# Kernel optimization log

Hardware: AMD Instinct MI355X
Metric: run time of the kernel (lower is better)

Reference implementation:

```python
import jax, jax.numpy as jnp
import numpy as np

H = 12           # num heads
ALPHA = 0.8      # mixing coefficient
OT_EPS = 1.0     # Sinkhorn epsilon
MAX_ITER = 50    # Sinkhorn iterations (reference runs full loop; torch may early-exit after convergence)
NEG = -1e9


def _l2norm(x, eps=1e-12):
    # matches torch.nn.functional.normalize(dim=-1)
    n = jnp.sqrt(jnp.sum(x * x, axis=-1, keepdims=True))
    return x / jnp.maximum(n, eps)


def setup_inputs() -> dict:
    rng = jax.random.key(0)
    ks = jax.random.split(rng, 12)
    B, L, D = 2, 2048, 768
    dk = D // H
    f = jnp.float32
    return {
        "query": jax.random.normal(ks[0], (B, L, D), dtype=f),
        "key": jax.random.normal(ks[1], (B, L, D), dtype=f),
        "short": jax.random.normal(ks[2], (B, H, L, L), dtype=f),
        "aspect": jax.random.normal(ks[3], (B, D), dtype=f),
        "mask": jnp.ones((B, 1, L), dtype=jnp.int32),
        "Wq": jax.random.normal(ks[4], (D, D), dtype=f) * (1.0 / np.sqrt(D)),
        "bq": jax.random.normal(ks[5], (D,), dtype=f) * 0.02,
        "Wk": jax.random.normal(ks[6], (D, D), dtype=f) * (1.0 / np.sqrt(D)),
        "bk": jax.random.normal(ks[7], (D,), dtype=f) * 0.02,
        "w_mu": jax.random.normal(ks[8], (dk, 1), dtype=f) * (1.0 / np.sqrt(dk)),
        "b_mu": jax.random.normal(ks[9], (1,), dtype=f) * 0.02,
        "bias_m": jax.random.normal(ks[10], (1,), dtype=f) * 0.02,
    }


def _forward(query, key, short, aspect, mask, Wq, bq, Wk, bk, w_mu, b_mu, bias_m):
    B, L, D = query.shape
    dk = D // H

    # unprojected head-split representations
    seq_h = query.reshape(B, L, H, dk).transpose(0, 2, 1, 3)       # [B,H,L,dk]
    asp_h = aspect.reshape(B, 1, H, dk).transpose(0, 2, 1, 3)      # [B,H,1,dk]

    m = mask[:, None, :, :]                                        # [B,1,1,L]

    q = (query @ Wq + bq).reshape(B, L, H, dk).transpose(0, 2, 1, 3)  # [B,H,L,dk]
    k = (key @ Wk + bk).reshape(B, L, H, dk).transpose(0, 2, 1, 3)    # [B,H,L,dk]

    scores = jnp.einsum('bhld,bhmd->bhlm', q, k) / np.sqrt(dk).astype(np.float32)
    scores = jnp.where(m == 0, NEG, scores)
    attn = jax.nn.softmax(scores + short, axis=-1)                 # [B,H,L,L]
    sentence_attn_output = jnp.einsum('bhlm,bhmd->bhld', attn, seq_h)

    # ---- Sinkhorn OT attention ----
    cos = jnp.sum(_l2norm(seq_h) * _l2norm(asp_h), axis=-1, keepdims=True)  # [B,H,L,1]
    cost = 1.0 - cos
    mu_logits = seq_h @ w_mu + b_mu                                # [B,H,L,1]
    m_t = jnp.transpose(m, (0, 1, 3, 2))                           # [B,1,L,1]
    mu_logits = jnp.where(m_t == 0, NEG, mu_logits)
    mu = jax.nn.softmax(mu_logits, axis=-2)                        # [B,H,L,1]
    nu = jax.nn.softmax(asp_h @ w_mu + b_mu, axis=-2)              # [B,H,1,1] (== 1)

    K = jnp.exp(-cost / OT_EPS)                                    # [B,H,L,1]

    def step(uv, _):
        u, v = uv
        u = mu / (K * v + 1e-8)                                    # K@v for [L,1]@[1,1]
        v = nu / (jnp.sum(K * u, axis=-2, keepdims=True) + 1e-8)   # K^T@u
        return (u, v), None

    (u, v), _ = jax.lax.scan(step, (jnp.ones_like(mu), jnp.ones_like(nu)), None, length=MAX_ITER)
    pi = u * K * v                                                 # [B,H,L,1]

    aspect_aware_rep = pi * seq_h                                  # [B,H,L,dk]
    out = ALPHA * sentence_attn_output + (1.0 - ALPHA) * aspect_aware_rep + bias_m
    return out                                                     # [B,H,L,dk]


def reference(query, key, short, aspect, mask, Wq, bq, Wk, bk, w_mu, b_mu, bias_m):
    return _forward(query, key, short, aspect, mask, Wq, bq, Wk, bk, w_mu, b_mu, bias_m)
```

## Files before the change

### kernel.cpp

```cpp
#include <hip/hip_runtime.h>
#include <math.h>

constexpr int NB = 2;
constexpr int NH = 12;
constexpr int SL = 2048;
constexpr int DM = 768;
constexpr int DK = 64;

typedef short s16x8 __attribute__((ext_vector_type(8)));
typedef float f32x4 __attribute__((ext_vector_type(4)));

__device__ inline unsigned short f2bf(float f) {
    unsigned int x = __float_as_uint(f);
    unsigned int r = (x + 0x7fffu + ((x >> 16) & 1u)) >> 16;
    return (unsigned short)r;
}
__device__ inline unsigned int pk2(float a, float b) {
    return (unsigned int)f2bf(a) | ((unsigned int)f2bf(b) << 16);
}

__global__ __launch_bounds__(256) void wt_cast(
    const float* __restrict__ W, unsigned short* __restrict__ Wt)
{
    __shared__ float t[64][65];
    const int k0 = blockIdx.x * 64, n0 = blockIdx.y * 64;
    const int tid = threadIdx.x;
    const int r = tid >> 2;
    const int c0 = (tid & 3) * 16;
#pragma unroll
    for (int j = 0; j < 4; ++j) {
        float4 v = *reinterpret_cast<const float4*>(
            &W[(size_t)(k0 + r) * DM + n0 + c0 + j * 4]);
        t[r][c0 + j*4 + 0] = v.x; t[r][c0 + j*4 + 1] = v.y;
        t[r][c0 + j*4 + 2] = v.z; t[r][c0 + j*4 + 3] = v.w;
    }
    __syncthreads();
    const int nr = tid >> 2, kc = (tid & 3) * 16;
    unsigned int o[8];
#pragma unroll
    for (int j = 0; j < 8; ++j)
        o[j] = pk2(t[kc + 2*j][nr], t[kc + 2*j + 1][nr]);
    unsigned short* dst = &Wt[(size_t)(n0 + nr) * DM + k0 + kc];
    uint4 a; a.x = o[0]; a.y = o[1]; a.z = o[2]; a.w = o[3];
    uint4 b; b.x = o[4]; b.y = o[5]; b.z = o[6]; b.w = o[7];
    *reinterpret_cast<uint4*>(dst) = a;
    *reinterpret_cast<uint4*>(dst + 8) = b;
}

__global__ __launch_bounds__(256) void proj_mfma(
    const float* __restrict__ X, const unsigned short* __restrict__ Wt,
    const float* __restrict__ bias, unsigned short* __restrict__ outw)
{
    __shared__ unsigned short Al[64 * 64];
    __shared__ unsigned short Bl[64 * 64];
    const int n0 = blockIdx.x * 64;
    const int m0 = blockIdx.y * 64;
    const int tid = threadIdx.x;
    const int w = tid >> 6, lane = tid & 63;
    const int lq = lane & 15, g = lane >> 4;
    const int msub = (w & 1) * 32, nsub = (w >> 1) * 32;

    const int srow = tid >> 2;
    const int sc = tid & 3;

    f32x4 acc[2][2];
#pragma unroll
    for (int i = 0; i < 2; ++i)
#pragma unroll
        for (int j = 0; j < 2; ++j) acc[i][j] = f32x4{0.f, 0.f, 0.f, 0.f};

    for (int k0 = 0; k0 < DM; k0 += 64) {
        const float* xp = &X[(size_t)(m0 + srow) * DM + k0 + sc * 8];
        float4 x0 = *reinterpret_cast<const float4*>(xp);
        float4 x1 = *reinterpret_cast<const float4*>(xp + 4);
        float4 x2 = *reinterpret_cast<const float4*>(xp + 32);
        float4 x3 = *reinterpret_cast<const float4*>(xp + 36);
        const unsigned short* wp = &Wt[(size_t)(n0 + srow) * DM + k0 + sc * 8];
        uint4 w0 = *reinterpret_cast<const uint4*>(wp);
        uint4 w1 = *reinterpret_cast<const uint4*>(wp + 32);
        __syncthreads();
        uint4 pa0, pa1;
        pa0.x = pk2(x0.x, x0.y); pa0.y = pk2(x0.z, x0.w);
        pa0.z = pk2(x1.x, x1.y); pa0.w = pk2(x1.z, x1.w);
        pa1.x = pk2(x2.x, x2.y); pa1.y = pk2(x2.z, x2.w);
        pa1.z = pk2(x3.x, x3.y); pa1.w = pk2(x3.z, x3.w);
        const int sw0 = (sc ^ (srow & 7)) << 3;
        const int sw1 = ((sc + 4) ^ (srow & 7)) << 3;
        *reinterpret_cast<uint4*>(&Al[srow * 64 + sw0]) = pa0;
        *reinterpret_cast<uint4*>(&Al[srow * 64 + sw1]) = pa1;
        *reinterpret_cast<uint4*>(&Bl[srow * 64 + sw0]) = w0;
        *reinterpret_cast<uint4*>(&Bl[srow * 64 + sw1]) = w1;
        __syncthreads();
#pragma unroll
        for (int ks = 0; ks < 2; ++ks) {
            s16x8 af[2], bfm[2];
#pragma unroll
            for (int ci = 0; ci < 2; ++ci) {
                const int row = nsub + ci * 16 + lq;
                af[ci] = *reinterpret_cast<const s16x8*>(
                    &Bl[row * 64 + (((4*ks + g) ^ (row & 7)) << 3)]);
            }
#pragma unroll
            for (int mi = 0; mi < 2; ++mi) {
                const int row = msub + mi * 16 + lq;
                bfm[mi] = *reinterpret_cast<const s16x8*>(
                    &Al[row * 64 + (((4*ks + g) ^ (row & 7)) << 3)]);
            }
#pragma unroll
            for (int ci = 0; ci < 2; ++ci)
#pragma unroll
                for (int mi = 0; mi < 2; ++mi)
                    acc[ci][mi] = __builtin_amdgcn_mfma_f32_16x16x32_bf16(
                        af[ci], bfm[mi], acc[ci][mi], 0, 0, 0);
        }
    }

    const int hh = blockIdx.x;
#pragma unroll
    for (int ci = 0; ci < 2; ++ci) {
        const int db = nsub + ci * 16 + g * 4;
        const float4 b4 = *reinterpret_cast<const float4*>(&bias[n0 + db]);
#pragma unroll
        for (int mi = 0; mi < 2; ++mi) {
            const int m = m0 + msub + mi * 16 + lq;
            const int b = m >> 11, l = m & 2047;
            uint2 uv;
            uv.x = pk2(acc[ci][mi][0] + b4.x, acc[ci][mi][1] + b4.y);
            uv.y = pk2(acc[ci][mi][2] + b4.z, acc[ci][mi][3] + b4.w);
            *reinterpret_cast<uint2*>(
                &outw[(((size_t)b * NH + hh) * SL + l) * DK + db]) = uv;
        }
    }
}

__device__ inline float block_sum(float v, float* red, int tid)
{
    __syncthreads();
#pragma unroll
    for (int o = 32; o > 0; o >>= 1) v += __shfl_down(v, o, 64);
    if ((tid & 63) == 0) red[tid >> 6] = v;
    __syncthreads();
    return red[0] + red[1] + red[2] + red[3];
}
__device__ inline float block_max(float v, float* red, int tid)
{
    __syncthreads();
#pragma unroll
    for (int o = 32; o > 0; o >>= 1) v = fmaxf(v, __shfl_down(v, o, 64));
    if ((tid & 63) == 0) red[tid >> 6] = v;
    __syncthreads();
    return fmaxf(fmaxf(red[0], red[1]), fmaxf(red[2], red[3]));
}

__global__ __launch_bounds__(256) void pi_kernel(
    const float* __restrict__ query, const float* __restrict__ aspect,
    const float* __restrict__ w_mu, const float* __restrict__ b_mu,
    float* __restrict__ pi_ws)
{
    const int bh = blockIdx.x;
    const int b = bh / NH, h = bh % NH;
    const int tid = threadIdx.x;

    __shared__ float red[4];
    __shared__ float wmu_s[DK];
    __shared__ float asp_s[DK];
    if (tid < DK) {
        wmu_s[tid] = w_mu[tid];
        asp_s[tid] = aspect[(size_t)b * DM + h * DK + tid];
    }
    __syncthreads();

    float an = 0.f;
#pragma unroll
    for (int d = 0; d < DK; ++d) an += asp_s[d] * asp_s[d];
    an = fmaxf(sqrtf(an), 1e-12f);

    float logit[8], Kv[8];
#pragma unroll
    for (int i = 0; i < 8; ++i) {
        const int l = tid + i * 256;
        const float4* x = reinterpret_cast<const float4*>(
            &query[((size_t)b * SL + l) * DM + h * DK]);
        float dot = 0.f, nn = 0.f, cs = 0.f;
#pragma unroll
        for (int d4 = 0; d4 < 16; ++d4) {
            const float4 xv = x[d4];
            dot += xv.x * wmu_s[d4*4+0] + xv.y * wmu_s[d4*4+1]
                 + xv.z * wmu_s[d4*4+2] + xv.w * wmu_s[d4*4+3];
            nn  += xv.x*xv.x + xv.y*xv.y + xv.z*xv.z + xv.w*xv.w;
            cs  += xv.x * asp_s[d4*4+0] + xv.y * asp_s[d4*4+1]
                 + xv.z * asp_s[d4*4+2] + xv.w * asp_s[d4*4+3];
        }
        const float n1 = fmaxf(sqrtf(nn), 1e-12f);
        const float cosv = cs / (n1 * an);
        logit[i] = dot + b_mu[0];
        Kv[i] = __expf(cosv - 1.0f);
    }

    float mx = logit[0];
#pragma unroll
    for (int i = 1; i < 8; ++i) mx = fmaxf(mx, logit[i]);
    const float gmax = block_max(mx, red, tid);

    float es[8]; float ps = 0.f;
#pragma unroll
    for (int i = 0; i < 8; ++i) { es[i] = __expf(logit[i] - gmax); ps += es[i]; }
    const float gsum = block_sum(ps, red, tid);

    float mu[8];
#pragma unroll
    for (int i = 0; i < 8; ++i) mu[i] = es[i] / gsum;

    float v = 1.f;
    float u[8] = {};
    for (int it = 0; it < 50; ++it) {
        float part = 0.f;
#pragma unroll
        for (int i = 0; i < 8; ++i) {
            u[i] = mu[i] / (Kv[i] * v + 1e-8f);
            part += Kv[i] * u[i];
        }
        const float S = block_sum(part, red, tid);
        v = 1.f / (S + 1e-8f);
    }

#pragma unroll
    for (int i = 0; i < 8; ++i) {
        const int l = tid + i * 256;
        pi_ws[(size_t)bh * SL + l] = u[i] * Kv[i] * v;
    }
}

__global__ __launch_bounds__(256) void flash_mfma(
    const unsigned short* __restrict__ q_ws,
    const unsigned short* __restrict__ k_ws,
    const float* __restrict__ query, const float* __restrict__ shortb,
    const float* __restrict__ pi_ws, const float* __restrict__ bias_m,
    float* __restrict__ out)
{
    __shared__ unsigned short Kl[64 * 64];
    __shared__ unsigned short Vt[64 * 64];

    const int bid = blockIdx.x;
    const int wg = (bid & 7) * 96 + (bid >> 3);
    const int bh = wg >> 5;
    const int qt = wg & 31;
    const int b = bh / NH, h = bh % NH;
    const int l0 = qt * 64;
    const int tid = threadIdx.x;
    const int w = tid >> 6, lane = tid & 63;
    const int lq = lane & 15, g = lane >> 4;
    const int qrow = l0 + w * 16 + lq;

    s16x8 qf0, qf1;
    {
        const unsigned short* qp = &q_ws[((size_t)bh * SL + qrow) * DK + g * 8];
        qf0 = *reinterpret_cast<const s16x8*>(qp);
        qf1 = *reinterpret_cast<const s16x8*>(qp + 32);
    }

    f32x4 acc[4];
#pragma unroll
    for (int d = 0; d < 4; ++d) acc[d] = f32x4{0.f, 0.f, 0.f, 0.f};
    float m_run = -1e30f, l_run = 0.f;

    const float* pshort = shortb + ((size_t)bh * SL + qrow) * SL;

    const int skey = tid >> 2, sc = tid & 3;
    const unsigned short* kgp =
        &k_ws[((size_t)bh * SL) * DK + skey * DK + sc * 8];
    unsigned short* kw0 = &Kl[skey * 64 + (((sc    ) ^ (skey & 7)) << 3)];
    unsigned short* kw1 = &Kl[skey * 64 + (((sc + 4) ^ (skey & 7)) << 3)];
    const int vkey = (tid & 31) * 2, vd0 = (tid >> 5) * 8;
    const float* vgp = &query[((size_t)b * SL) * DM + h * DK + vd0];

    auto stage = [&](int kt) {
        const unsigned short* kp = kgp + (size_t)kt * DK;
        uint4 ka = *reinterpret_cast<const uint4*>(kp);
        uint4 kb = *reinterpret_cast<const uint4*>(kp + 32);
        const float* vp = vgp + (size_t)(kt + vkey) * DM;
        float4 f0 = *reinterpret_cast<const float4*>(vp);
        float4 f1 = *reinterpret_cast<const float4*>(vp + 4);
        float4 f2 = *reinterpret_cast<const float4*>(vp + DM);
        float4 f3 = *reinterpret_cast<const float4*>(vp + DM + 4);
        __syncthreads();
        *reinterpret_cast<uint4*>(kw0) = ka;
        *reinterpret_cast<uint4*>(kw1) = kb;
        const float a0[8] = {f0.x,f0.y,f0.z,f0.w,f1.x,f1.y,f1.z,f1.w};
        const float a1[8] = {f2.x,f2.y,f2.z,f2.w,f3.x,f3.y,f3.z,f3.w};
#pragma unroll
        for (int j = 0; j < 8; ++j) {
            const int d = vd0 + j;
            *reinterpret_cast<unsigned int*>(
                &Vt[d * 64 + (vkey ^ ((d & 7) << 3))]) = pk2(a0[j], a1[j]);
        }
        __syncthreads();
    };

    auto compute = [&](const float4* shp) {
        f32x4 st[4];
#pragma unroll
        for (int s = 0; s < 4; ++s) {
            const int row = s * 16 + lq;
            const s16x8 ka0 = *reinterpret_cast<const s16x8*>(
                &Kl[row * 64 + (((g    ) ^ (row & 7)) << 3)]);
            const s16x8 ka1 = *reinterpret_cast<const s16x8*>(
                &Kl[row * 64 + (((4 + g) ^ (row & 7)) << 3)]);
            f32x4 c = {0.f, 0.f, 0.f, 0.f};
            c = __builtin_amdgcn_mfma_f32_16x16x32_bf16(ka0, qf0, c, 0, 0, 0);
            c = __builtin_amdgcn_mfma_f32_16x16x32_bf16(ka1, qf1, c, 0, 0, 0);
            st[s] = c;
        }
        float p[4][4];
        float tmax = -1e30f;
#pragma unroll
        for (int s = 0; s < 4; ++s) {
            const float* s4 = reinterpret_cast<const float*>(&shp[s]);
#pragma unroll
            for (int r = 0; r < 4; ++r) {
                const float sc_ = st[s][r] * 0.125f + s4[r];
                p[s][r] = sc_;
                tmax = fmaxf(tmax, sc_);
            }
        }
        tmax = fmaxf(tmax, __shfl_xor(tmax, 16));
        tmax = fmaxf(tmax, __shfl_xor(tmax, 32));
        const float m_new = fmaxf(m_run, tmax);
        const float alpha = __expf(m_run - m_new);
        float psum = 0.f;
#pragma unroll
        for (int s = 0; s < 4; ++s)
#pragma unroll
            for (int r = 0; r < 4; ++r) {
                const float e = __expf(p[s][r] - m_new);
                p[s][r] = e; psum += e;
            }
        psum += __shfl_xor(psum, 16);
        psum += __shfl_xor(psum, 32);
        l_run = l_run * alpha + psum;
        m_run = m_new;
#pragma unroll
        for (int d = 0; d < 4; ++d) acc[d] *= alpha;

        unsigned int wpk[4][2];
#pragma unroll
        for (int s = 0; s < 4; ++s) {
            wpk[s][0] = pk2(p[s][0], p[s][1]);
            wpk[s][1] = pk2(p[s][2], p[s][3]);
        }
        const int src_lo = lq + ((g & 1) << 5);
        s16x8 pf[2];
#pragma unroll
        for (int ks = 0; ks < 2; ++ks) {
            union { unsigned int u[4]; s16x8 v; } cv;
#pragma unroll
            for (int i = 0; i < 4; ++i) {
                const int srcl = src_lo + ((i >> 1) << 4);
                const unsigned int tA =
                    (unsigned int)__shfl((int)wpk[2*ks][i & 1], srcl);
                const unsigned int tB =
                    (unsigned int)__shfl((int)wpk[2*ks + 1][i & 1], srcl);
                cv.u[i] = (g >> 1) ? tB : tA;
            }
            pf[ks] = cv.v;
        }
#pragma unroll
        for (int d = 0; d < 4; ++d) {
            const int row = d * 16 + lq;
            const s16x8 va0 = *reinterpret_cast<const s16x8*>(
                &Vt[row * 64 + (((g    ) ^ (row & 7)) << 3)]);
            const s16x8 va1 = *reinterpret_cast<const s16x8*>(
                &Vt[row * 64 + (((4 + g) ^ (row & 7)) << 3)]);
            acc[d] = __builtin_amdgcn_mfma_f32_16x16x32_bf16(va0, pf[0], acc[d], 0, 0, 0);
            acc[d] = __builtin_amdgcn_mfma_f32_16x16x32_bf16(va1, pf[1], acc[d], 0, 0, 0);
        }
    };

    float4 shpA[4], shpB[4];
#pragma unroll
    for (int s = 0; s < 4; ++s)
        shpA[s] = *reinterpret_cast<const float4*>(&pshort[s * 16 + g * 4]);

    for (int kt = 0; kt < SL; kt += 128) {
        stage(kt);
        {
            const int ktn = kt + 64;
#pragma unroll
            for (int s = 0; s < 4; ++s)
                shpB[s] = *reinterpret_cast<const float4*>(
                    &pshort[ktn + s * 16 + g * 4]);
        }
        compute(shpA);
        stage(kt + 64);
        {
            const int ktn = (kt + 128) & (SL - 1);
#pragma unroll
            for (int s = 0; s < 4; ++s)
                shpA[s] = *reinterpret_cast<const float4*>(
                    &pshort[ktn + s * 16 + g * 4]);
        }
        compute(shpB);
    }

    const float inv = 1.0f / l_run;
    const float pv = pi_ws[(size_t)bh * SL + qrow];
    const float bm = bias_m[0];
    const float* seq = &query[((size_t)b * SL + qrow) * DM + h * DK];
    float* op = &out[((size_t)bh * SL + qrow) * DK];
#pragma unroll
    for (int d = 0; d < 4; ++d) {
        const int dbase = d * 16 + g * 4;
        const float4 sq = *reinterpret_cast<const float4*>(&seq[dbase]);
        float4 o;
        o.x = 0.8f * acc[d][0] * inv + 0.2f * pv * sq.x + bm;
        o.y = 0.8f * acc[d][1] * inv + 0.2f * pv * sq.y + bm;
        o.z = 0.8f * acc[d][2] * inv + 0.2f * pv * sq.z + bm;
        o.w = 0.8f * acc[d][3] * inv + 0.2f * pv * sq.w + bm;
        *reinterpret_cast<float4*>(&op[dbase]) = o;
    }
}

extern "C" void kernel_launch(void* const* d_in, const int* in_sizes, int n_in,
                              void* d_out, int out_size, void* d_ws, size_t ws_size,
                              hipStream_t stream)
{
    (void)in_sizes; (void)n_in; (void)out_size; (void)ws_size;
    const float* query  = (const float*)d_in[0];
    const float* key    = (const float*)d_in[1];
    const float* shortb = (const float*)d_in[2];
    const float* aspect = (const float*)d_in[3];
    const float* Wq     = (const float*)d_in[5];
    const float* bq     = (const float*)d_in[6];
    const float* Wk     = (const float*)d_in[7];
    const float* bk     = (const float*)d_in[8];
    const float* w_mu   = (const float*)d_in[9];
    const float* b_mu   = (const float*)d_in[10];
    const float* bias_m = (const float*)d_in[11];
    float* out = (float*)d_out;

    unsigned short* Wqt  = (unsigned short*)d_ws;
    unsigned short* Wkt  = Wqt + (size_t)DM * DM;
    unsigned short* q_ws = Wkt + (size_t)DM * DM;
    unsigned short* k_ws = q_ws + (size_t)NB * NH * SL * DK;
    float* pi_ws = (float*)(k_ws + (size_t)NB * NH * SL * DK);

    wt_cast<<<dim3(12, 12), 256, 0, stream>>>(Wq, Wqt);
    wt_cast<<<dim3(12, 12), 256, 0, stream>>>(Wk, Wkt);
    proj_mfma<<<dim3(12, 64), 256, 0, stream>>>(query, Wqt, bq, q_ws);
    proj_mfma<<<dim3(12, 64), 256, 0, stream>>>(key,   Wkt, bk, k_ws);
    pi_kernel<<<NB * NH, 256, 0, stream>>>(query, aspect, w_mu, b_mu, pi_ws);
    flash_mfma<<<768, 256, 0, stream>>>(q_ws, k_ws, query, shortb,
                                        pi_ws, bias_m, out);
}
```

Measured before the change: 685.0 us.

## Merge launches, deepen projection K tile, single-wave Sinkhorn, prefetch flash K/V

The Q and K weight casts and projections are each merged into a single launch using a z grid dimension, and the projection GEMM now stages 128-wide K slices, halving the number of barriers. The Sinkhorn loop in pi_kernel is reformulated so that one wavefront per block computes the sum with shuffle reductions and hardware reciprocals, removing block-wide barriers from every iteration. The flash kernel now issues the global loads for the next K/V tile before the current tile's compute, splitting load and LDS write so that memory latency overlaps with MFMA work. The trade-offs are higher register pressure and slightly approximate reciprocals.

```diff
diff --git a/kernel.cpp b/kernel.cpp
--- a/kernel.cpp
+++ b/kernel.cpp
@@ -20,8 +20,11 @@
 }
 
 __global__ __launch_bounds__(256) void wt_cast(
-    const float* __restrict__ W, unsigned short* __restrict__ Wt)
-{
+    const float* __restrict__ Wq, const float* __restrict__ Wk,
+    unsigned short* __restrict__ Wtq, unsigned short* __restrict__ Wtk)
+{
+    const float* W = blockIdx.z ? Wk : Wq;
+    unsigned short* Wt = blockIdx.z ? Wtk : Wtq;
     __shared__ float t[64][65];
     const int k0 = blockIdx.x * 64, n0 = blockIdx.y * 64;
     const int tid = threadIdx.x;
@@ -48,11 +51,19 @@
 }
 
 __global__ __launch_bounds__(256) void proj_mfma(
-    const float* __restrict__ X, const unsigned short* __restrict__ Wt,
-    const float* __restrict__ bias, unsigned short* __restrict__ outw)
-{
-    __shared__ unsigned short Al[64 * 64];
-    __shared__ unsigned short Bl[64 * 64];
+    const float* __restrict__ Xq, const float* __restrict__ Xk,
+    const unsigned short* __restrict__ Wtq, const unsigned short* __restrict__ Wtk,
+    const float* __restrict__ bq, const float* __restrict__ bk,
+    unsigned short* __restrict__ oq, unsigned short* __restrict__ ok)
+{
+    const int z = blockIdx.z;
+    const float* X = z ? Xk : Xq;
+    const unsigned short* Wt = z ? Wtk : Wtq;
+    const float* bias = z ? bk : bq;
+    unsigned short* outw = z ? ok : oq;
+
+    __shared__ unsigned short Al[64 * 128];
+    __shared__ unsigned short Bl[64 * 128];
     const int n0 = blockIdx.x * 64;
     const int m0 = blockIdx.y * 64;
     const int tid = threadIdx.x;
@@ -69,42 +80,65 @@
 #pragma unroll
         for (int j = 0; j < 2; ++j) acc[i][j] = f32x4{0.f, 0.f, 0.f, 0.f};
 
-    for (int k0 = 0; k0 < DM; k0 += 64) {
+    for (int k0 = 0; k0 < DM; k0 += 128) {
         const float* xp = &X[(size_t)(m0 + srow) * DM + k0 + sc * 8];
         float4 x0 = *reinterpret_cast<const float4*>(xp);
         float4 x1 = *reinterpret_cast<const float4*>(xp + 4);
         float4 x2 = *reinterpret_cast<const float4*>(xp + 32);
         float4 x3 = *reinterpret_cast<const float4*>(xp + 36);
+        float4 x4 = *reinterpret_cast<const float4*>(xp + 64);
+        float4 x5 = *reinterpret_cast<const float4*>(xp + 68);
+        float4 x6 = *reinterpret_cast<const float4*>(xp + 96);
+        float4 x7 = *reinterpret_cast<const float4*>(xp + 100);
         const unsigned short* wp = &Wt[(size_t)(n0 + srow) * DM + k0 + sc * 8];
         uint4 w0 = *reinterpret_cast<const uint4*>(wp);
         uint4 w1 = *reinterpret_cast<const uint4*>(wp + 32);
+        uint4 w2 = *reinterpret_cast<const uint4*>(wp + 64);
+        uint4 w3 = *reinterpret_cast<const uint4*>(wp + 96);
         __syncthreads();
-        uint4 pa0, pa1;
-        pa0.x = pk2(x0.x, x0.y); pa0.y = pk2(x0.z, x0.w);
-        pa0.z = pk2(x1.x, x1.y); pa0.w = pk2(x1.z, x1.w);
-        pa1.x = pk2(x2.x, x2.y); pa1.y = pk2(x2.z, x2.w);
-        pa1.z = pk2(x3.x, x3.y); pa1.w = pk2(x3.z, x3.w);
-        const int sw0 = (sc ^ (srow & 7)) << 3;
-        const int sw1 = ((sc + 4) ^ (srow & 7)) << 3;
-        *reinterpret_cast<uint4*>(&Al[srow * 64 + sw0]) = pa0;
-        *reinterpret_cast<uint4*>(&Al[srow * 64 + sw1]) = pa1;
-        *reinterpret_cast<uint4*>(&Bl[srow * 64 + sw0]) = w0;
-        *reinterpret_cast<uint4*>(&Bl[srow * 64 + sw1]) = w1;
+        {
+            uint4 pa; pa.x = pk2(x0.x, x0.y); pa.y = pk2(x0.z, x0.w);
+            pa.z = pk2(x1.x, x1.y); pa.w = pk2(x1.z, x1.w);
+            const int sw = ((sc     ) ^ (srow & 7)) << 3;
+            *reinterpret_cast<uint4*>(&Al[srow * 128 + sw]) = pa;
+            *reinterpret_cast<uint4*>(&Bl[srow * 128 + sw]) = w0;
+        }
+        {
+            uint4 pa; pa.x = pk2(x2.x, x2.y); pa.y = pk2(x2.z, x2.w);
+            pa.z = pk2(x3.x, x3.y); pa.w = pk2(x3.z, x3.w);
+            const int sw = ((sc +  4) ^ (srow & 7)) << 3;
+            *reinterpret_cast<uint4*>(&Al[srow * 128 + sw]) = pa;
+            *reinterpret_cast<uint4*>(&Bl[srow * 128 + sw]) = w1;
+        }
+        {
+            uint4 pa; pa.x = pk2(x4.x, x4.y); pa.y = pk2(x4.z, x4.w);
+            pa.z = pk2(x5.x, x5.y); pa.w = pk2(x5.z, x5.w);
+            const int sw = ((sc +  8) ^ (srow & 7)) << 3;
+            *reinterpret_cast<uint4*>(&Al[srow * 128 + sw]) = pa;
+            *reinterpret_cast<uint4*>(&Bl[srow * 128 + sw]) = w2;
+        }
+        {
+            uint4 pa; pa.x = pk2(x6.x, x6.y); pa.y = pk2(x6.z, x6.w);
+            pa.z = pk2(x7.x, x7.y); pa.w = pk2(x7.z, x7.w);
+            const int sw = ((sc + 12) ^ (srow & 7)) << 3;
+            *reinterpret_cast<uint4*>(&Al[srow * 128 + sw]) = pa;
+            *reinterpret_cast<uint4*>(&Bl[srow * 128 + sw]) = w3;
+        }
         __syncthreads();
 #pragma unroll
-        for (int ks = 0; ks < 2; ++ks) {
+        for (int ks = 0; ks < 4; ++ks) {
             s16x8 af[2], bfm[2];
 #pragma unroll
             for (int ci = 0; ci < 2; ++ci) {
                 const int row = nsub + ci * 16 + lq;
                 af[ci] = *reinterpret_cast<const s16x8*>(
-                    &Bl[row * 64 + (((4*ks + g) ^ (row & 7)) << 3)]);
+                    &Bl[row * 128 + (((ks*4 + g) ^ (row & 7)) << 3)]);
             }
 #pragma unroll
             for (int mi = 0; mi < 2; ++mi) {
                 const int row = msub + mi * 16 + lq;
                 bfm[mi] = *reinterpret_cast<const s16x8*>(
-                    &Al[row * 64 + (((4*ks + g) ^ (row & 7)) << 3)]);
+                    &Al[row * 128 + (((ks*4 + g) ^ (row & 7)) << 3)]);
             }
 #pragma unroll
             for (int ci = 0; ci < 2; ++ci)
@@ -164,6 +198,8 @@
     __shared__ float red[4];
     __shared__ float wmu_s[DK];
     __shared__ float asp_s[DK];
+    __shared__ float a_s[64 * 33];
+    __shared__ float b_s[64 * 33];
     if (tid < DK) {
         wmu_s[tid] = w_mu[tid];
         asp_s[tid] = aspect[(size_t)b * DM + h * DK + tid];
@@ -211,23 +247,38 @@
 #pragma unroll
     for (int i = 0; i < 8; ++i) mu[i] = es[i] / gsum;
 
-    float v = 1.f;
-    float u[8] = {};
-    for (int it = 0; it < 50; ++it) {
-        float part = 0.f;
-#pragma unroll
-        for (int i = 0; i < 8; ++i) {
-            u[i] = mu[i] / (Kv[i] * v + 1e-8f);
-            part += Kv[i] * u[i];
-        }
-        const float S = block_sum(part, red, tid);
-        v = 1.f / (S + 1e-8f);
-    }
-
 #pragma unroll
     for (int i = 0; i < 8; ++i) {
         const int l = tid + i * 256;
-        pi_ws[(size_t)bh * SL + l] = u[i] * Kv[i] * v;
+        a_s[(l & 63) * 33 + (l >> 6)] = mu[i] * Kv[i];
+        b_s[(l & 63) * 33 + (l >> 6)] = Kv[i];
+    }
+    __syncthreads();
+
+    const int lane = tid & 63;
+    float av[32], bv[32];
+#pragma unroll
+    for (int j = 0; j < 32; ++j) {
+        av[j] = a_s[lane * 33 + j];
+        bv[j] = b_s[lane * 33 + j];
+    }
+    float v = 1.f, vp = 1.f;
+    for (int it = 0; it < 50; ++it) {
+        vp = v;
+        float S = 0.f;
+#pragma unroll
+        for (int j = 0; j < 32; ++j)
+            S += av[j] * __builtin_amdgcn_rcpf(fmaf(bv[j], vp, 1e-8f));
+#pragma unroll
+        for (int o = 1; o < 64; o <<= 1) S += __shfl_xor(S, o);
+        v = __builtin_amdgcn_rcpf(S + 1e-8f);
+    }
+
+#pragma unroll
+    for (int i = 0; i < 8; ++i) {
+        const int l = tid + i * 256;
+        pi_ws[(size_t)bh * SL + l] =
+            mu[i] * Kv[i] * v * __builtin_amdgcn_rcpf(fmaf(Kv[i], vp, 1e-8f));
     }
 }
 
@@ -274,16 +325,20 @@
     const int vkey = (tid & 31) * 2, vd0 = (tid >> 5) * 8;
     const float* vgp = &query[((size_t)b * SL) * DM + h * DK + vd0];
 
-    auto stage = [&](int kt) {
+    auto loadKV = [&](int kt, uint4& ka, uint4& kb,
+                      float4& f0, float4& f1, float4& f2, float4& f3) {
         const unsigned short* kp = kgp + (size_t)kt * DK;
-        uint4 ka = *reinterpret_cast<const uint4*>(kp);
-        uint4 kb = *reinterpret_cast<const uint4*>(kp + 32);
+        ka = *reinterpret_cast<const uint4*>(kp);
+        kb = *reinterpret_cast<const uint4*>(kp + 32);
         const float* vp = vgp + (size_t)(kt + vkey) * DM;
-        float4 f0 = *reinterpret_cast<const float4*>(vp);
-        float4 f1 = *reinterpret_cast<const float4*>(vp + 4);
-        float4 f2 = *reinterpret_cast<const float4*>(vp + DM);
-        float4 f3 = *reinterpret_cast<const float4*>(vp + DM + 4);
-        __syncthreads();
+        f0 = *reinterpret_cast<const float4*>(vp);
+        f1 = *reinterpret_cast<const float4*>(vp + 4);
+        f2 = *reinterpret_cast<const float4*>(vp + DM);
+        f3 = *reinterpret_cast<const float4*>(vp + DM + 4);
+    };
+    auto writeKV = [&](const uint4& ka, const uint4& kb,
+                       const float4& f0, const float4& f1,
+                       const float4& f2, const float4& f3) {
         *reinterpret_cast<uint4*>(kw0) = ka;
         *reinterpret_cast<uint4*>(kw1) = kb;
         const float a0[8] = {f0.x,f0.y,f0.z,f0.w,f1.x,f1.y,f1.z,f1.w};
@@ -294,7 +349,6 @@
             *reinterpret_cast<unsigned int*>(
                 &Vt[d * 64 + (vkey ^ ((d & 7) << 3))]) = pk2(a0[j], a1[j]);
         }
-        __syncthreads();
     };
 
     auto compute = [&](const float4* shp) {
@@ -376,30 +430,41 @@
         }
     };
 
+    uint4 kaA, kbA, kaB, kbB;
+    float4 vA0, vA1, vA2, vA3, vB0, vB1, vB2, vB3;
+    loadKV(0, kaA, kbA, vA0, vA1, vA2, vA3);
+    writeKV(kaA, kbA, vA0, vA1, vA2, vA3);
+    __syncthreads();
+
     float4 shpA[4], shpB[4];
 #pragma unroll
     for (int s = 0; s < 4; ++s)
         shpA[s] = *reinterpret_cast<const float4*>(&pshort[s * 16 + g * 4]);
 
     for (int kt = 0; kt < SL; kt += 128) {
-        stage(kt);
-        {
-            const int ktn = kt + 64;
-#pragma unroll
-            for (int s = 0; s < 4; ++s)
-                shpB[s] = *reinterpret_cast<const float4*>(
-                    &pshort[ktn + s * 16 + g * 4]);
-        }
+        loadKV(kt + 64, kaB, kbB, vB0, vB1, vB2, vB3);
+#pragma unroll
+        for (int s = 0; s < 4; ++s)
+            shpB[s] = *reinterpret_cast<const float4*>(
+                &pshort[kt + 64 + s * 16 + g * 4]);
         compute(shpA);
-        stage(kt + 64);
-        {
-            const int ktn = (kt + 128) & (SL - 1);
+        __syncthreads();
+        writeKV(kaB, kbB, vB0, vB1, vB2, vB3);
+        __syncthreads();
+        const bool lastit = (kt + 128 >= SL);
+        if (!lastit) {
+            loadKV(kt + 128, kaA, kbA, vA0, vA1, vA2, vA3);
 #pragma unroll
             for (int s = 0; s < 4; ++s)
                 shpA[s] = *reinterpret_cast<const float4*>(
-                    &pshort[ktn + s * 16 + g * 4]);
+                    &pshort[kt + 128 + s * 16 + g * 4]);
         }
         compute(shpB);
+        if (!lastit) {
+            __syncthreads();
+            writeKV(kaA, kbA, vA0, vA1, vA2, vA3);
+            __syncthreads();
+        }
     }
 
     const float inv = 1.0f / l_run;
@@ -444,10 +509,9 @@
     unsigned short* k_ws = q_ws + (size_t)NB * NH * SL * DK;
     float* pi_ws = (float*)(k_ws + (size_t)NB * NH * SL * DK);
 
-    wt_cast<<<dim3(12, 12), 256, 0, stream>>>(Wq, Wqt);
-    wt_cast<<<dim3(12, 12), 256, 0, stream>>>(Wk, Wkt);
-    proj_mfma<<<dim3(12, 64), 256, 0, stream>>>(query, Wqt, bq, q_ws);
-    proj_mfma<<<dim3(12, 64), 256, 0, stream>>>(key,   Wkt, bk, k_ws);
+    wt_cast<<<dim3(12, 12, 2), 256, 0, stream>>>(Wq, Wk, Wqt, Wkt);
+    proj_mfma<<<dim3(12, 64, 2), 256, 0, stream>>>(
+        query, key, Wqt, Wkt, bq, bk, q_ws, k_ws);
     pi_kernel<<<NB * NH, 256, 0, stream>>>(query, aspect, w_mu, b_mu, pi_ws);
     flash_mfma<<<768, 256, 0, stream>>>(q_ws, k_ws, query, shortb,
                                         pi_ws, bias_m, out);
```

After: 689.8 us. About the same (+0.7%).
